# Optimization experiments

Measured on AMD Instinct MI355X. Metric: run time of the kernel, lower is better.

The kernel has to match this reference:

```python
import jax, jax.numpy as jnp
import numpy as np

KEY_SIZE = 512
QUERY_SIZE = 512
ATTN_SIZE = 128
B, Q, K = 4, 256, 1024


def setup_inputs() -> dict:
    key0 = jax.random.key(0)
    ks = jax.random.split(key0, 9)
    s_k = 1.0 / np.sqrt(KEY_SIZE)
    s_q = 1.0 / np.sqrt(QUERY_SIZE)
    s_a = 1.0 / np.sqrt(ATTN_SIZE)
    return {
        "key": jax.random.normal(ks[0], (B, K, KEY_SIZE), jnp.float32),
        "query": jax.random.normal(ks[1], (B, Q, QUERY_SIZE), jnp.float32),
        "value": jax.random.normal(ks[2], (B, K, KEY_SIZE), jnp.float32),
        # nn.Linear params (PyTorch layout: W [out,in]); uniform(-1/sqrt(in), 1/sqrt(in))
        "Wk": jax.random.uniform(ks[3], (ATTN_SIZE, KEY_SIZE), jnp.float32, -s_k, s_k),
        "bk": jax.random.uniform(ks[4], (ATTN_SIZE,), jnp.float32, -s_k, s_k),
        "Wq": jax.random.uniform(ks[5], (ATTN_SIZE, QUERY_SIZE), jnp.float32, -s_q, s_q),
        "bq": jax.random.uniform(ks[6], (ATTN_SIZE,), jnp.float32, -s_q, s_q),
        "Wa": jax.random.uniform(ks[7], (ATTN_SIZE,), jnp.float32, -s_a, s_a),
        "ba": jax.random.uniform(ks[8], (), jnp.float32, -s_a, s_a),
    }


def reference(key, query, value, Wk, bk, Wq, bq, Wa, ba):
    # Rank-3 query branch of MLPAttention.forward (return_value=True, return_score=False)
    h1 = jnp.einsum('bqd,ad->bqa', query, Wq) + bq          # [B,Q,A]
    h2 = jnp.einsum('bkd,ad->bka', key, Wk) + bk            # [B,K,A]
    h = jax.nn.relu(h1[:, :, None, :] + h2[:, None, :, :])  # [B,Q,K,A] big intermediate
    logits = jnp.einsum('bqka,a->bqk', h, Wa) + ba          # attention_layer -> [B,Q,K]
    score = jax.nn.softmax(logits, axis=2)                  # softmax over klen
    out = jnp.einsum('bqk,bkd->bqd', score, value)          # weighted sum over K
    return out
```

## Files before the change

### kernel.cpp

```cpp
#include <hip/hip_runtime.h>
#include <hip/hip_bf16.h>
#include <math.h>

#define NB 4
#define NQ 256
#define NK 1024
#define ND 512
#define NA 128

#define OFFB_H1 0u
#define OFFB_H2 524288u
#define OFFB_SC 2621440u
#define OFFB_VT 4718592u

#define PROJ_BLKS 80

typedef __attribute__((ext_vector_type(8))) short short8;
typedef __attribute__((ext_vector_type(8))) unsigned short ushort8_t;
typedef __attribute__((ext_vector_type(4))) float f32x4;

static __device__ __forceinline__ ushort f2bf(float x) {
    __hip_bfloat16 h = __float2bfloat16(x);
    return *reinterpret_cast<ushort*>(&h);
}

static __device__ __forceinline__ unsigned swz(int row, int o) {
    return (unsigned)(row * 256 + (o ^ ((row & 7) << 4) ^ (((o >> 7) & 1) << 5)));
}

__global__ __launch_bounds__(256) void k_proj_vt(
    const float* __restrict__ query, const float* __restrict__ key,
    const float* __restrict__ value,
    const float* __restrict__ Wq, const float* __restrict__ bq,
    const float* __restrict__ Wk, const float* __restrict__ bk,
    float* __restrict__ h1, float* __restrict__ h2,
    __hip_bfloat16* __restrict__ vt)
{
    __shared__ __align__(16) ushort smem[24576];
    char* sbytes = (char*)smem;
    const int tid = threadIdx.x;
    const int bid = blockIdx.x;

    if (bid < PROJ_BLKS) {
        const int r0 = bid * 64;
        const bool isQ = r0 < NB * NQ;
        const float* X    = isQ ? query + (size_t)r0 * ND : key + (size_t)(r0 - NB * NQ) * ND;
        const float* W    = isQ ? Wq : Wk;
        const float* bias = isQ ? bq : bk;
        float* hout       = isQ ? h1 + (size_t)r0 * NA : h2 + (size_t)(r0 - NB * NQ) * NA;

        const int wave = tid >> 6, lane = tid & 63;
        const int l15 = lane & 15, lkb = (lane >> 4) * 16;

        f32x4 acc[8] = {};

        for (int kc = 0; kc < ND; kc += 128) {
            __syncthreads();
            {
                const int row = tid >> 2, kg = (tid & 3) * 32;
                const float* src = X + (size_t)row * ND + kc + kg;
                #pragma unroll
                for (int j = 0; j < 4; ++j) {
                    const float4 v0 = *(const float4*)(src + j * 8);
                    const float4 v1 = *(const float4*)(src + j * 8 + 4);
                    ushort8_t o;
                    o[0] = f2bf(v0.x); o[1] = f2bf(v0.y); o[2] = f2bf(v0.z); o[3] = f2bf(v0.w);
                    o[4] = f2bf(v1.x); o[5] = f2bf(v1.y); o[6] = f2bf(v1.z); o[7] = f2bf(v1.w);
                    *(ushort8_t*)(sbytes + swz(row, kg * 2 + j * 16)) = o;
                }
            }
            {
                const int row = tid >> 1, kg = (tid & 1) * 64;
                const float* src = W + (size_t)row * ND + kc + kg;
                #pragma unroll
                for (int j = 0; j < 8; ++j) {
                    const float4 v0 = *(const float4*)(src + j * 8);
                    const float4 v1 = *(const float4*)(src + j * 8 + 4);
                    ushort8_t o;
                    o[0] = f2bf(v0.x); o[1] = f2bf(v0.y); o[2] = f2bf(v0.z); o[3] = f2bf(v0.w);
                    o[4] = f2bf(v1.x); o[5] = f2bf(v1.y); o[6] = f2bf(v1.z); o[7] = f2bf(v1.w);
                    *(ushort8_t*)(sbytes + 16384 + swz(row, kg * 2 + j * 16)) = o;
                }
            }
            __syncthreads();
            #pragma unroll
            for (int kk = 0; kk < 4; ++kk) {
                const int arow = wave * 16 + l15;
                const short8 a = *(const short8*)(sbytes + swz(arow, kk * 64 + lkb));
                #pragma unroll
                for (int ct = 0; ct < 8; ++ct) {
                    const int bcol = ct * 16 + l15;
                    const short8 b = *(const short8*)(sbytes + 16384 + swz(bcol, kk * 64 + lkb));
                    acc[ct] = __builtin_amdgcn_mfma_f32_16x16x32_bf16(a, b, acc[ct], 0, 0, 0);
                }
            }
        }

        const int orow0 = wave * 16 + (lane >> 4) * 4;
        #pragma unroll
        for (int ct = 0; ct < 8; ++ct) {
            const int col = ct * 16 + l15;
            const float bb = bias[col];
            #pragma unroll
            for (int r = 0; r < 4; ++r)
                hout[(size_t)(orow0 + r) * NA + col] = acc[ct][r] + bb;
        }
    } else {
        ushort (*tile)[65] = (ushort (*)[65])smem;
        const int id = bid - PROJ_BLKS;
        const int kt = id & 15;
        const int dt = (id >> 4) & 7;
        const int b  = id >> 7;
        const int k0 = kt * 64, d0 = dt * 64;
        const int tr = tid >> 4, tc4 = (tid & 15) * 4;

        #pragma unroll
        for (int p = 0; p < 4; ++p) {
            const int r = p * 16 + tr;
            const float4 v = *(const float4*)(value + ((size_t)(b * NK + k0 + r)) * ND + d0 + tc4);
            tile[r][tc4 + 0] = f2bf(v.x); tile[r][tc4 + 1] = f2bf(v.y);
            tile[r][tc4 + 2] = f2bf(v.z); tile[r][tc4 + 3] = f2bf(v.w);
        }
        __syncthreads();
        ushort* vo = (ushort*)vt;
        #pragma unroll
        for (int p = 0; p < 4; ++p) {
            const int d = p * 16 + tr;
            ushort4 o;
            o.x = tile[tc4 + 0][d]; o.y = tile[tc4 + 1][d];
            o.z = tile[tc4 + 2][d]; o.w = tile[tc4 + 3][d];
            *(ushort4*)(vo + ((size_t)(b * ND + d0 + d)) * NK + k0 + tc4) = o;
        }
    }
}

__global__ __launch_bounds__(512) void k_logits_softmax(
    const float* __restrict__ h1, const float* __restrict__ h2,
    const float* __restrict__ Wa, __hip_bfloat16* __restrict__ score)
{
    __shared__ float redm[4][8];
    __shared__ float reds[4][8];
    const int tid = threadIdx.x;
    const int b = blockIdx.x >> 6;
    const int q0 = (blockIdx.x & 63) << 2;

    const float4* __restrict__ h2b = (const float4*)(h2 + (size_t)b * NK * NA);
    const float4* __restrict__ h1g = (const float4*)(h1 + (size_t)(b * NQ + q0) * NA);
    const float4* __restrict__ wag = (const float4*)Wa;

    float lg[4][2];
    #pragma unroll
    for (int c = 0; c < 2; ++c) {
        const int k = tid + c * 512;
        const float4* row = h2b + (size_t)k * 32;
        float s0 = 0.f, s1 = 0.f, s2 = 0.f, s3 = 0.f;
        #pragma unroll 8
        for (int a4 = 0; a4 < 32; ++a4) {
            const float4 hv = row[a4];
            const float4 wv = wag[a4];
            const float4 p0 = h1g[0 * 32 + a4];
            const float4 p1 = h1g[1 * 32 + a4];
            const float4 p2 = h1g[2 * 32 + a4];
            const float4 p3 = h1g[3 * 32 + a4];
            s0 = fmaf(wv.x, fmaxf(p0.x + hv.x, 0.f), s0);
            s0 = fmaf(wv.y, fmaxf(p0.y + hv.y, 0.f), s0);
            s0 = fmaf(wv.z, fmaxf(p0.z + hv.z, 0.f), s0);
            s0 = fmaf(wv.w, fmaxf(p0.w + hv.w, 0.f), s0);
            s1 = fmaf(wv.x, fmaxf(p1.x + hv.x, 0.f), s1);
            s1 = fmaf(wv.y, fmaxf(p1.y + hv.y, 0.f), s1);
            s1 = fmaf(wv.z, fmaxf(p1.z + hv.z, 0.f), s1);
            s1 = fmaf(wv.w, fmaxf(p1.w + hv.w, 0.f), s1);
            s2 = fmaf(wv.x, fmaxf(p2.x + hv.x, 0.f), s2);
            s2 = fmaf(wv.y, fmaxf(p2.y + hv.y, 0.f), s2);
            s2 = fmaf(wv.z, fmaxf(p2.z + hv.z, 0.f), s2);
            s2 = fmaf(wv.w, fmaxf(p2.w + hv.w, 0.f), s2);
            s3 = fmaf(wv.x, fmaxf(p3.x + hv.x, 0.f), s3);
            s3 = fmaf(wv.y, fmaxf(p3.y + hv.y, 0.f), s3);
            s3 = fmaf(wv.z, fmaxf(p3.z + hv.z, 0.f), s3);
            s3 = fmaf(wv.w, fmaxf(p3.w + hv.w, 0.f), s3);
        }
        lg[0][c] = s0; lg[1][c] = s1; lg[2][c] = s2; lg[3][c] = s3;
    }

    const int wv_ = tid >> 6, ln = tid & 63;
    float mq[4];
    #pragma unroll
    for (int q = 0; q < 4; ++q) {
        float m = fmaxf(lg[q][0], lg[q][1]);
        for (int off = 32; off > 0; off >>= 1) m = fmaxf(m, __shfl_xor(m, off));
        if (ln == 0) redm[q][wv_] = m;
    }
    __syncthreads();
    #pragma unroll
    for (int q = 0; q < 4; ++q) {
        float m = redm[q][0];
        #pragma unroll
        for (int w = 1; w < 8; ++w) m = fmaxf(m, redm[q][w]);
        mq[q] = m;
    }
    #pragma unroll
    for (int q = 0; q < 4; ++q) {
        float s = 0.f;
        #pragma unroll
        for (int c = 0; c < 2; ++c) { lg[q][c] = __expf(lg[q][c] - mq[q]); s += lg[q][c]; }
        for (int off = 32; off > 0; off >>= 1) s += __shfl_xor(s, off);
        if (ln == 0) reds[q][wv_] = s;
    }
    __syncthreads();
    #pragma unroll
    for (int q = 0; q < 4; ++q) {
        float s = reds[q][0];
        #pragma unroll
        for (int w = 1; w < 8; ++w) s += reds[q][w];
        const float inv = 1.f / s;
        __hip_bfloat16* so = score + (size_t)(b * NQ + q0 + q) * NK + tid;
        #pragma unroll
        for (int c = 0; c < 2; ++c) so[c * 512] = __float2bfloat16(lg[q][c] * inv);
    }
}

__global__ __launch_bounds__(256) void k_pv(
    const ushort* __restrict__ sc,
    const ushort* __restrict__ vt,
    float* __restrict__ out)
{
    const int tid = threadIdx.x;
    const int wave = tid >> 6, lane = tid & 63;
    const int wr = wave >> 1, wc = wave & 1;
    const int m0 = blockIdx.x * 32 + wr * 16;
    const int n0 = blockIdx.y * 64 + wc * 32;
    const int b  = blockIdx.z;
    const int l15 = lane & 15, lk = (lane >> 4) * 8;

    const ushort* arow  = sc + (size_t)(b * NQ + m0 + l15) * NK + lk;
    const ushort* b0row = vt + (size_t)(b * ND + n0 + l15) * NK + lk;
    const ushort* b1row = vt + (size_t)(b * ND + n0 + 16 + l15) * NK + lk;

    f32x4 acc0 = {0.f, 0.f, 0.f, 0.f}, acc1 = {0.f, 0.f, 0.f, 0.f};
    #pragma unroll 4
    for (int k = 0; k < NK; k += 32) {
        const short8 a  = *(const short8*)(arow + k);
        const short8 v0 = *(const short8*)(b0row + k);
        const short8 v1 = *(const short8*)(b1row + k);
        acc0 = __builtin_amdgcn_mfma_f32_16x16x32_bf16(a, v0, acc0, 0, 0, 0);
        acc1 = __builtin_amdgcn_mfma_f32_16x16x32_bf16(a, v1, acc1, 0, 0, 0);
    }

    const int orow = (lane >> 4) * 4;
    #pragma unroll
    for (int r = 0; r < 4; ++r) {
        float* po = out + (size_t)(b * NQ + m0 + orow + r) * ND + n0;
        po[l15]      = acc0[r];
        po[16 + l15] = acc1[r];
    }
}

extern "C" void kernel_launch(void* const* d_in, const int* in_sizes, int n_in,
                              void* d_out, int out_size, void* d_ws, size_t ws_size,
                              hipStream_t stream) {
    const float* key   = (const float*)d_in[0];
    const float* query = (const float*)d_in[1];
    const float* value = (const float*)d_in[2];
    const float* Wk    = (const float*)d_in[3];
    const float* bk    = (const float*)d_in[4];
    const float* Wq    = (const float*)d_in[5];
    const float* bq    = (const float*)d_in[6];
    const float* Wa    = (const float*)d_in[7];

    char* ws = (char*)d_ws;
    float* h1 = (float*)(ws + OFFB_H1);
    float* h2 = (float*)(ws + OFFB_H2);
    __hip_bfloat16* sc = (__hip_bfloat16*)(ws + OFFB_SC);
    __hip_bfloat16* vt = (__hip_bfloat16*)(ws + OFFB_VT);

    k_proj_vt<<<PROJ_BLKS + 512, 256, 0, stream>>>(query, key, value, Wq, bq, Wk, bk,
                                                   h1, h2, vt);
    k_logits_softmax<<<256, 512, 0, stream>>>(h1, h2, Wa, sc);
    k_pv<<<dim3(8, 8, 4), 256, 0, stream>>>((const ushort*)sc, (const ushort*)vt,
                                            (float*)d_out);
}
```

Before: 59.05 us.

## Use packed fp16 dot products for logits and shrink PV tiles

The projections h1/h2 and Wa are stored as fp16, and the logits inner loop uses packed half2 adds with relu written as (x+|x|) times 0.5*Wa, accumulated through fdot2 into fp32. This halves the memory traffic for h1/h2 and roughly halves the VALU instruction count in the dominant logits kernel. The PV kernel is also changed so each wave computes one 16x16 tile, and the grid is doubled for more parallelism. The cost is fp16 rounding of the projections and their sums, which could overflow or lose precision.

```diff
diff --git a/kernel.cpp b/kernel.cpp
--- a/kernel.cpp
+++ b/kernel.cpp
@@ -1,5 +1,6 @@
 #include <hip/hip_runtime.h>
 #include <hip/hip_bf16.h>
+#include <hip/hip_fp16.h>
 #include <math.h>
 
 #define NB 4
@@ -9,6 +10,7 @@
 #define NA 128
 
 #define OFFB_H1 0u
+#define OFFB_WA 262144u
 #define OFFB_H2 524288u
 #define OFFB_SC 2621440u
 #define OFFB_VT 4718592u
@@ -18,11 +20,18 @@
 typedef __attribute__((ext_vector_type(8))) short short8;
 typedef __attribute__((ext_vector_type(8))) unsigned short ushort8_t;
 typedef __attribute__((ext_vector_type(4))) float f32x4;
+typedef _Float16 half2v __attribute__((ext_vector_type(2)));
 
 static __device__ __forceinline__ ushort f2bf(float x) {
     __hip_bfloat16 h = __float2bfloat16(x);
     return *reinterpret_cast<ushort*>(&h);
 }
+static __device__ __forceinline__ half2v u2h(unsigned u) {
+    union { unsigned u; half2v h; } c; c.u = u; return c.h;
+}
+static __device__ __forceinline__ unsigned h2u(half2v h) {
+    union { half2v h; unsigned u; } c; c.h = h; return c.u;
+}
 
 static __device__ __forceinline__ unsigned swz(int row, int o) {
     return (unsigned)(row * 256 + (o ^ ((row & 7) << 4) ^ (((o >> 7) & 1) << 5)));
@@ -30,10 +39,10 @@
 
 __global__ __launch_bounds__(256) void k_proj_vt(
     const float* __restrict__ query, const float* __restrict__ key,
-    const float* __restrict__ value,
+    const float* __restrict__ value, const float* __restrict__ Wa,
     const float* __restrict__ Wq, const float* __restrict__ bq,
     const float* __restrict__ Wk, const float* __restrict__ bk,
-    float* __restrict__ h1, float* __restrict__ h2,
+    __half* __restrict__ h1, __half* __restrict__ h2, __half* __restrict__ wa16,
     __hip_bfloat16* __restrict__ vt)
 {
     __shared__ __align__(16) ushort smem[24576];
@@ -47,7 +56,7 @@
         const float* X    = isQ ? query + (size_t)r0 * ND : key + (size_t)(r0 - NB * NQ) * ND;
         const float* W    = isQ ? Wq : Wk;
         const float* bias = isQ ? bq : bk;
-        float* hout       = isQ ? h1 + (size_t)r0 * NA : h2 + (size_t)(r0 - NB * NQ) * NA;
+        __half* hout      = isQ ? h1 + (size_t)r0 * NA : h2 + (size_t)(r0 - NB * NQ) * NA;
 
         const int wave = tid >> 6, lane = tid & 63;
         const int l15 = lane & 15, lkb = (lane >> 4) * 16;
@@ -103,9 +112,12 @@
             const float bb = bias[col];
             #pragma unroll
             for (int r = 0; r < 4; ++r)
-                hout[(size_t)(orow0 + r) * NA + col] = acc[ct][r] + bb;
+                hout[(size_t)(orow0 + r) * NA + col] = __float2half(acc[ct][r] + bb);
         }
     } else {
+        if (bid == PROJ_BLKS && tid < NA)
+            wa16[tid] = __float2half(0.5f * Wa[tid]);
+
         ushort (*tile)[65] = (ushort (*)[65])smem;
         const int id = bid - PROJ_BLKS;
         const int kt = id & 15;
@@ -135,8 +147,8 @@
 }
 
 __global__ __launch_bounds__(512) void k_logits_softmax(
-    const float* __restrict__ h1, const float* __restrict__ h2,
-    const float* __restrict__ Wa, __hip_bfloat16* __restrict__ score)
+    const ushort* __restrict__ h1, const ushort* __restrict__ h2,
+    const ushort* __restrict__ wa16, __hip_bfloat16* __restrict__ score)
 {
     __shared__ float redm[4][8];
     __shared__ float reds[4][8];
@@ -144,40 +156,47 @@
     const int b = blockIdx.x >> 6;
     const int q0 = (blockIdx.x & 63) << 2;
 
-    const float4* __restrict__ h2b = (const float4*)(h2 + (size_t)b * NK * NA);
-    const float4* __restrict__ h1g = (const float4*)(h1 + (size_t)(b * NQ + q0) * NA);
-    const float4* __restrict__ wag = (const float4*)Wa;
+    const uint4* __restrict__ h2b = (const uint4*)(h2 + (size_t)b * NK * NA);
+    const uint4* __restrict__ h1g = (const uint4*)(h1 + (size_t)(b * NQ + q0) * NA);
+    const uint4* __restrict__ wag = (const uint4*)wa16;
 
     float lg[4][2];
     #pragma unroll
     for (int c = 0; c < 2; ++c) {
         const int k = tid + c * 512;
-        const float4* row = h2b + (size_t)k * 32;
+        const uint4* row = h2b + (size_t)k * 16;
         float s0 = 0.f, s1 = 0.f, s2 = 0.f, s3 = 0.f;
-        #pragma unroll 8
-        for (int a4 = 0; a4 < 32; ++a4) {
-            const float4 hv = row[a4];
-            const float4 wv = wag[a4];
-            const float4 p0 = h1g[0 * 32 + a4];
-            const float4 p1 = h1g[1 * 32 + a4];
-            const float4 p2 = h1g[2 * 32 + a4];
-            const float4 p3 = h1g[3 * 32 + a4];
-            s0 = fmaf(wv.x, fmaxf(p0.x + hv.x, 0.f), s0);
-            s0 = fmaf(wv.y, fmaxf(p0.y + hv.y, 0.f), s0);
-            s0 = fmaf(wv.z, fmaxf(p0.z + hv.z, 0.f), s0);
-            s0 = fmaf(wv.w, fmaxf(p0.w + hv.w, 0.f), s0);
-            s1 = fmaf(wv.x, fmaxf(p1.x + hv.x, 0.f), s1);
-            s1 = fmaf(wv.y, fmaxf(p1.y + hv.y, 0.f), s1);
-            s1 = fmaf(wv.z, fmaxf(p1.z + hv.z, 0.f), s1);
-            s1 = fmaf(wv.w, fmaxf(p1.w + hv.w, 0.f), s1);
-            s2 = fmaf(wv.x, fmaxf(p2.x + hv.x, 0.f), s2);
-            s2 = fmaf(wv.y, fmaxf(p2.y + hv.y, 0.f), s2);
-            s2 = fmaf(wv.z, fmaxf(p2.z + hv.z, 0.f), s2);
-            s2 = fmaf(wv.w, fmaxf(p2.w + hv.w, 0.f), s2);
-            s3 = fmaf(wv.x, fmaxf(p3.x + hv.x, 0.f), s3);
-            s3 = fmaf(wv.y, fmaxf(p3.y + hv.y, 0.f), s3);
-            s3 = fmaf(wv.z, fmaxf(p3.z + hv.z, 0.f), s3);
-            s3 = fmaf(wv.w, fmaxf(p3.w + hv.w, 0.f), s3);
+        #pragma unroll
+        for (int i = 0; i < 16; ++i) {
+            const uint4 hv = row[i];
+            const uint4 wv = wag[i];
+            const uint4 p0 = h1g[0 * 16 + i];
+            const uint4 p1 = h1g[1 * 16 + i];
+            const uint4 p2 = h1g[2 * 16 + i];
+            const uint4 p3 = h1g[3 * 16 + i];
+            const unsigned hu[4] = {hv.x, hv.y, hv.z, hv.w};
+            const unsigned wu[4] = {wv.x, wv.y, wv.z, wv.w};
+            const unsigned q0u[4] = {p0.x, p0.y, p0.z, p0.w};
+            const unsigned q1u[4] = {p1.x, p1.y, p1.z, p1.w};
+            const unsigned q2u[4] = {p2.x, p2.y, p2.z, p2.w};
+            const unsigned q3u[4] = {p3.x, p3.y, p3.z, p3.w};
+            #pragma unroll
+            for (int j = 0; j < 4; ++j) {
+                const half2v hh = u2h(hu[j]);
+                const half2v ww = u2h(wu[j]);
+                {   half2v x = u2h(q0u[j]) + hh;
+                    half2v y = x + u2h(h2u(x) & 0x7FFF7FFFu);
+                    s0 = __builtin_amdgcn_fdot2(y, ww, s0, false); }
+                {   half2v x = u2h(q1u[j]) + hh;
+                    half2v y = x + u2h(h2u(x) & 0x7FFF7FFFu);
+                    s1 = __builtin_amdgcn_fdot2(y, ww, s1, false); }
+                {   half2v x = u2h(q2u[j]) + hh;
+                    half2v y = x + u2h(h2u(x) & 0x7FFF7FFFu);
+                    s2 = __builtin_amdgcn_fdot2(y, ww, s2, false); }
+                {   half2v x = u2h(q3u[j]) + hh;
+                    half2v y = x + u2h(h2u(x) & 0x7FFF7FFFu);
+                    s3 = __builtin_amdgcn_fdot2(y, ww, s3, false); }
+            }
         }
         lg[0][c] = s0; lg[1][c] = s1; lg[2][c] = s2; lg[3][c] = s3;
     }
@@ -226,33 +245,26 @@
 {
     const int tid = threadIdx.x;
     const int wave = tid >> 6, lane = tid & 63;
-    const int wr = wave >> 1, wc = wave & 1;
-    const int m0 = blockIdx.x * 32 + wr * 16;
-    const int n0 = blockIdx.y * 64 + wc * 32;
+    const int m0 = blockIdx.x * 16;
+    const int n0 = blockIdx.y * 64 + wave * 16;
     const int b  = blockIdx.z;
     const int l15 = lane & 15, lk = (lane >> 4) * 8;
 
-    const ushort* arow  = sc + (size_t)(b * NQ + m0 + l15) * NK + lk;
-    const ushort* b0row = vt + (size_t)(b * ND + n0 + l15) * NK + lk;
-    const ushort* b1row = vt + (size_t)(b * ND + n0 + 16 + l15) * NK + lk;
-
-    f32x4 acc0 = {0.f, 0.f, 0.f, 0.f}, acc1 = {0.f, 0.f, 0.f, 0.f};
-    #pragma unroll 4
+    const ushort* arow = sc + (size_t)(b * NQ + m0 + l15) * NK + lk;
+    const ushort* brow = vt + (size_t)(b * ND + n0 + l15) * NK + lk;
+
+    f32x4 acc = {0.f, 0.f, 0.f, 0.f};
+    #pragma unroll 8
     for (int k = 0; k < NK; k += 32) {
-        const short8 a  = *(const short8*)(arow + k);
-        const short8 v0 = *(const short8*)(b0row + k);
-        const short8 v1 = *(const short8*)(b1row + k);
-        acc0 = __builtin_amdgcn_mfma_f32_16x16x32_bf16(a, v0, acc0, 0, 0, 0);
-        acc1 = __builtin_amdgcn_mfma_f32_16x16x32_bf16(a, v1, acc1, 0, 0, 0);
+        const short8 a = *(const short8*)(arow + k);
+        const short8 v = *(const short8*)(brow + k);
+        acc = __builtin_amdgcn_mfma_f32_16x16x32_bf16(a, v, acc, 0, 0, 0);
     }
 
     const int orow = (lane >> 4) * 4;
     #pragma unroll
-    for (int r = 0; r < 4; ++r) {
-        float* po = out + (size_t)(b * NQ + m0 + orow + r) * ND + n0;
-        po[l15]      = acc0[r];
-        po[16 + l15] = acc1[r];
-    }
+    for (int r = 0; r < 4; ++r)
+        out[(size_t)(b * NQ + m0 + orow + r) * ND + n0 + l15] = acc[r];
 }
 
 extern "C" void kernel_launch(void* const* d_in, const int* in_sizes, int n_in,
@@ -268,14 +280,16 @@
     const float* Wa    = (const float*)d_in[7];
 
     char* ws = (char*)d_ws;
-    float* h1 = (float*)(ws + OFFB_H1);
-    float* h2 = (float*)(ws + OFFB_H2);
+    __half* h1 = (__half*)(ws + OFFB_H1);
+    __half* wa16 = (__half*)(ws + OFFB_WA);
+    __half* h2 = (__half*)(ws + OFFB_H2);
     __hip_bfloat16* sc = (__hip_bfloat16*)(ws + OFFB_SC);
     __hip_bfloat16* vt = (__hip_bfloat16*)(ws + OFFB_VT);
 
-    k_proj_vt<<<PROJ_BLKS + 512, 256, 0, stream>>>(query, key, value, Wq, bq, Wk, bk,
-                                                   h1, h2, vt);
-    k_logits_softmax<<<256, 512, 0, stream>>>(h1, h2, Wa, sc);
-    k_pv<<<dim3(8, 8, 4), 256, 0, stream>>>((const ushort*)sc, (const ushort*)vt,
-                                            (float*)d_out);
-}
+    k_proj_vt<<<PROJ_BLKS + 512, 256, 0, stream>>>(query, key, value, Wa,
+                                                   Wq, bq, Wk, bk, h1, h2, wa16, vt);
+    k_logits_softmax<<<256, 512, 0, stream>>>((const ushort*)h1, (const ushort*)h2,
+                                              (const ushort*)wa16, sc);
+    k_pv<<<dim3(16, 8, 4), 256, 0, stream>>>((const ushort*)sc, (const ushort*)vt,
+                                             (float*)d_out);
+}
```

Measured after the change: 62.94 us. 1.07x slower.
